# Performance work log

Hardware: AMD Instinct MI355X
Metric: run time of the kernel (lower is better)

Reference implementation:

```python
import jax, jax.numpy as jnp
import numpy as np

EMBED_DIM = 256
NUM_HEADS = 8
HEAD_DIM = EMBED_DIM // NUM_HEADS
SCALE = HEAD_DIM ** -0.5  # note: scale uses head_dim even though attention is over full D
EPS = 1e-12  # torch F.normalize eps


def setup_inputs() -> dict:
    key = jax.random.key(0)
    k1, k2, k3 = jax.random.split(key, 3)
    B, Nq, Nk, D = 4, 4096, 4096, EMBED_DIM
    return {
        "query": jax.random.normal(k1, (B, Nq, D), dtype=jnp.float32),
        "key": jax.random.normal(k2, (B, Nk, D), dtype=jnp.float32),
        "value": jax.random.normal(k3, (B, Nk, D), dtype=jnp.float32),
    }


def _l2_normalize(x):
    # matches torch.nn.functional.normalize(x, dim=-1): x / max(||x||, eps)
    n = jnp.linalg.norm(x, axis=-1, keepdims=True)
    return x / jnp.maximum(n, EPS)


def reference(query, key, value):
    q = _l2_normalize(query)          # (B, Nq, D)
    k = _l2_normalize(key)            # (B, Nk, D)
    scores = jnp.einsum("bqd,bkd->bqk", q, k) * SCALE  # (B, Nq, Nk) cosine sims
    attn = jax.nn.softmax(scores, axis=-1)
    return jnp.einsum("bqk,bkd->bqd", attn, value)     # (B, Nq, D)
```

## Files before the change

kernel.cpp:

```cpp
#include <hip/hip_runtime.h>


#define NQ 4096
#define DIM 256
#define NROWS 16384
#define BM 64
#define BN 64
#define KSPLIT 2
#define NITER 32
#define PSTRIDE 68

typedef __attribute__((ext_vector_type(8))) short bf16x8;
typedef __attribute__((ext_vector_type(4))) float f32x4;
typedef __attribute__((ext_vector_type(16))) float f32x16;

__device__ __forceinline__ unsigned short f2bf(float f) {
  unsigned int u = __float_as_uint(f);
  u += 0x7fffu + ((u >> 16) & 1u);
  return (unsigned short)(u >> 16);
}

__device__ __forceinline__ float bf2f(unsigned short h) {
  return __uint_as_float((unsigned int)h << 16);
}

__device__ __forceinline__ unsigned int pack2bf(float a, float b) {
  unsigned int ua = __float_as_uint(a) + 0x8000u;
  unsigned int ub = __float_as_uint(b) + 0x8000u;
  return __builtin_amdgcn_perm(ub, ua, 0x07060302u);
}

__device__ __forceinline__ void gload16(const void* g, void* l) {
  __builtin_amdgcn_global_load_lds(
      (const __attribute__((address_space(1))) unsigned int*)g,
      (__attribute__((address_space(3))) unsigned int*)l, 16, 0, 0);
}

__global__ __launch_bounds__(256) void prep(
    const float* __restrict__ K, const float* __restrict__ V,
    unsigned short* __restrict__ Kfm, unsigned short* __restrict__ Vfm)
{
  __shared__ unsigned short vt[32 * 264];
  const int blk = blockIdx.x, tid = threadIdx.x;
  const int wave = tid >> 6, lane = tid & 63;
  if (blk < 512) {
    const int kt2 = blk;
    const int kt = kt2 >> 1, h = kt2 & 1;
    #pragma unroll
    for (int i = 0; i < 8; i++) {
      const int r = wave*8 + i;
      float4 v = *(const float4*)(K + ((size_t)kt2*32 + r) * DIM + lane * 4);
      float ss = v.x*v.x + v.y*v.y + v.z*v.z + v.w*v.w;
      #pragma unroll
      for (int off = 1; off < 64; off <<= 1) ss += __shfl_xor(ss, off, 64);
      float scale = 1.0f / fmaxf(sqrtf(ss), 1e-12f);
      ushort4 o;
      o.x = f2bf(v.x*scale); o.y = f2bf(v.y*scale);
      o.z = f2bf(v.z*scale); o.w = f2bf(v.w*scale);
      *(ushort4*)(vt + r*264 + lane*4) = o;
    }
    __syncthreads();
    #pragma unroll
    for (int s = 0; s < 4; s++) {
      const int ch = tid + 256*s;
      const int c = ch >> 5, r = ch & 31;
      const int n = h*32 + r;
      bf16x8 val = *(const bf16x8*)(vt + r*264 + c*8);
      *(bf16x8*)(Kfm + (size_t)kt*16384 + (size_t)(c*64 + n)*8) = val;
    }
  } else {
    const int NS = blk - 512;
    #pragma unroll
    for (int i = 0; i < 4; i++) {
      const int e = tid + 256*i;
      const int nl = e >> 6, d = (e & 63) * 4;
      float4 v = *(const float4*)(V + ((size_t)NS*16 + nl)*DIM + d);
      ushort4 o;
      o.x = f2bf(v.x); o.y = f2bf(v.y); o.z = f2bf(v.z); o.w = f2bf(v.w);
      *(ushort4*)(vt + nl*264 + d) = o;
    }
    __syncthreads();
    #pragma unroll
    for (int i = 0; i < 2; i++) {
      const int ch = tid + 256*i;
      const int db = ch >> 6, ln = ch & 63;
      const int row0 = (ln >> 5) * 8, dd = db*32 + (ln & 31);
      ushort4 a, b;
      a.x = vt[(row0+0)*264 + dd]; a.y = vt[(row0+1)*264 + dd];
      a.z = vt[(row0+2)*264 + dd]; a.w = vt[(row0+3)*264 + dd];
      b.x = vt[(row0+4)*264 + dd]; b.y = vt[(row0+5)*264 + dd];
      b.z = vt[(row0+6)*264 + dd]; b.w = vt[(row0+7)*264 + dd];
      size_t base = ((size_t)(NS*8 + db)*64 + ln)*8;
      *(ushort4*)(Vfm + base)     = a;
      *(ushort4*)(Vfm + base + 4) = b;
    }
  }
}

__global__ __launch_bounds__(256, 2) void attn(
    const float* __restrict__ Qg,
    const unsigned short* __restrict__ Kfm,
    const unsigned short* __restrict__ Vfm,
    unsigned short* __restrict__ Opart, float* __restrict__ lpart)
{
  __shared__ unsigned short Klds[32 * 64 * 8];
  __shared__ unsigned short Plds[BM * PSTRIDE];

  const int tid = threadIdx.x, wave = tid >> 6, lane = tid & 63;
  const int l15 = lane & 15, l4 = lane >> 4;
  const int blk = blockIdx.x;
  const int g = blk & 7, qt = blk >> 3;
  const int b = g >> 1, ks = g & 1;
  const int Rq0 = b*NQ + qt*BM;
  const int n0base = b*NQ + ks*(NQ/KSPLIT);
  const int mi = wave & 1, ni = wave >> 1;

  {
    unsigned short* Qlds = Klds;
    #pragma unroll
    for (int i = 0; i < 16; i++) {
      const int r = wave*16 + i;
      float4 v = *(const float4*)(Qg + (size_t)(Rq0 + r)*DIM + lane*4);
      float ss = v.x*v.x + v.y*v.y + v.z*v.z + v.w*v.w;
      #pragma unroll
      for (int off = 1; off < 64; off <<= 1) ss += __shfl_xor(ss, off, 64);
      float scale = (0.17677669529663687f * 1.4426950408889634f)
                    / fmaxf(sqrtf(ss), 1e-12f);
      ushort4 o;
      o.x = f2bf(v.x*scale); o.y = f2bf(v.y*scale);
      o.z = f2bf(v.z*scale); o.w = f2bf(v.w*scale);
      *(ushort4*)(Qlds + r*DIM + lane*4) = o;
    }
  }
  __syncthreads();

  bf16x8 qf[2][8];
  #pragma unroll
  for (int mt = 0; mt < 2; mt++) {
    const unsigned short* qrow = Klds + (mi*32 + mt*16 + l15)*DIM + l4*8;
    #pragma unroll
    for (int kg = 0; kg < 8; kg++)
      qf[mt][kg] = *(const bf16x8*)(qrow + kg*32);
  }
  __syncthreads();

  f32x16 oacc[2][2] = {};
  float lacc[2] = {};

  auto stage = [&](int kt) {
    const unsigned short* src = Kfm + (size_t)((n0base + kt*BN) >> 6) * (32*64*8);
    #pragma unroll
    for (int jj = 0; jj < 4; jj++) {
      const int c = wave*8 + jj*2;
      gload16(src + (size_t)c*512 + lane*8,     Klds + (size_t)c*512);
      gload16(src + (size_t)(c+1)*512 + lane*8, Klds + (size_t)(c+1)*512);
    }
  };

  stage(0);

  for (int kt = 0; kt < NITER; kt++) {
    __syncthreads();

    f32x4 sacc[2][2] = {};
    #pragma unroll
    for (int kg = 0; kg < 8; kg++) {
      bf16x8 kf[2];
      #pragma unroll
      for (int nt = 0; nt < 2; nt++) {
        const int nrow = ni*32 + nt*16 + l15;
        const int c = kg*4 + l4;
        kf[nt] = *(const bf16x8*)(Klds + ((size_t)(c*64 + nrow))*8);
      }
      #pragma unroll
      for (int nt = 0; nt < 2; nt++)
        #pragma unroll
        for (int mt = 0; mt < 2; mt++)
          sacc[nt][mt] = __builtin_amdgcn_mfma_f32_16x16x32_bf16(
              kf[nt], qf[mt][kg], sacc[nt][mt], 0, 0, 0);
    }

    #pragma unroll
    for (int nt = 0; nt < 2; nt++)
      #pragma unroll
      for (int mt = 0; mt < 2; mt++) {
        float p0 = __builtin_amdgcn_exp2f(sacc[nt][mt][0]);
        float p1 = __builtin_amdgcn_exp2f(sacc[nt][mt][1]);
        float p2 = __builtin_amdgcn_exp2f(sacc[nt][mt][2]);
        float p3 = __builtin_amdgcn_exp2f(sacc[nt][mt][3]);
        lacc[mt] += (p0 + p1) + (p2 + p3);
        uint2 pk;
        pk.x = pack2bf(p0, p1);
        pk.y = pack2bf(p2, p3);
        const int m = mi*32 + mt*16 + l15;
        const int n = ni*32 + nt*16 + 4*l4;
        *(uint2*)(Plds + m*PSTRIDE + n) = pk;
      }

    __syncthreads();

    if (kt + 1 < NITER) stage(kt + 1);

    const int NB0 = (n0base + kt*BN) >> 4;
    #pragma unroll
    for (int kstep = 0; kstep < 4; kstep++) {
      bf16x8 pf[2], vf[2];
      #pragma unroll
      for (int mt2 = 0; mt2 < 2; mt2++)
        pf[mt2] = *(const bf16x8*)(Plds + (mt2*32 + (lane & 31))*PSTRIDE
                                   + kstep*16 + 8*(lane >> 5));
      #pragma unroll
      for (int dt = 0; dt < 2; dt++) {
        const int db = wave*2 + dt;
        vf[dt] = *(const bf16x8*)(Vfm + ((size_t)((NB0 + kstep)*8 + db)*64 + lane)*8);
      }
      #pragma unroll
      for (int mt2 = 0; mt2 < 2; mt2++)
        #pragma unroll
        for (int dt = 0; dt < 2; dt++)
          oacc[mt2][dt] = __builtin_amdgcn_mfma_f32_32x32x16_bf16(
              pf[mt2], vf[dt], oacc[mt2][dt], 0, 0, 0);
    }
  }

  #pragma unroll
  for (int mt = 0; mt < 2; mt++) {
    float s = lacc[mt];
    s += __shfl_xor(s, 16, 64);
    s += __shfl_xor(s, 32, 64);
    if (l4 == 0)
      lpart[(size_t)(ks*2 + ni)*NROWS + Rq0 + mi*32 + mt*16 + l15] = s;
  }

  #pragma unroll
  for (int mt2 = 0; mt2 < 2; mt2++)
    #pragma unroll
    for (int dt = 0; dt < 2; dt++)
      #pragma unroll
      for (int reg = 0; reg < 16; reg++) {
        const int m = mt2*32 + 4*(lane >> 5) + (reg & 3) + 8*(reg >> 2);
        const int d = wave*64 + dt*32 + (lane & 31);
        Opart[((size_t)(ks*NROWS + Rq0 + m))*DIM + d] = f2bf(oacc[mt2][dt][reg]);
      }
}

__global__ __launch_bounds__(256) void combine(
    const unsigned short* __restrict__ Opart, const float* __restrict__ lpart,
    float* __restrict__ out)
{
  const size_t idx = (size_t)blockIdx.x*256 + threadIdx.x;
  const size_t e = idx*4;
  const int R = (int)(e >> 8);
  ushort4 o0 = *(const ushort4*)(Opart + e);
  ushort4 o1 = *(const ushort4*)(Opart + (size_t)NROWS*DIM + e);
  float ls = lpart[R] + lpart[NROWS + R] + lpart[2*NROWS + R] + lpart[3*NROWS + R];
  float inv = 1.0f / ls;
  float4 o;
  o.x = (bf2f(o0.x) + bf2f(o1.x))*inv;
  o.y = (bf2f(o0.y) + bf2f(o1.y))*inv;
  o.z = (bf2f(o0.z) + bf2f(o1.z))*inv;
  o.w = (bf2f(o0.w) + bf2f(o1.w))*inv;
  *(float4*)(out + e) = o;
}

extern "C" void kernel_launch(void* const* d_in, const int* in_sizes, int n_in,
                              void* d_out, int out_size, void* d_ws, size_t ws_size,
                              hipStream_t stream) {
  const float* Q = (const float*)d_in[0];
  const float* K = (const float*)d_in[1];
  const float* V = (const float*)d_in[2];
  char* ws = (char*)d_ws;
  unsigned short* Kfm   = (unsigned short*)(ws);
  unsigned short* Vfm   = (unsigned short*)(ws + 8388608);
  unsigned short* Opart = (unsigned short*)(ws + 16777216);
  float* lpart = (float*)(ws + 33554432);

  prep<<<1536, 256, 0, stream>>>(K, V, Kfm, Vfm);
  attn<<<512, 256, 0, stream>>>(Q, Kfm, Vfm, Opart, lpart);
  combine<<<4096, 256, 0, stream>>>(Opart, lpart, (float*)d_out);
}
```

Baseline: 174.6 us.

## Halve query tile to 32 rows, raise occupancy, add MFMA priority hints

Shrinks the query tile from 64 to 32 rows per block, doubling the grid to 1024 blocks and cutting the accumulator and Q-fragment registers so launch bounds can request 4 blocks per CU. Each wave now handles one 16-row slice of scores and one 32-row output tile. s_setprio is raised around the MFMA sequences to favour matrix issue among co-resident waves. The aim is better latency hiding and CU fill. The cost is that every K/V tile is reloaded twice as often per query row, which doubles K/V traffic from L2 and HBM and lowers MFMA work per LDS load.

New measurement: 192.1 us. +10.0%, slower.

```diff
diff --git a/kernel.cpp b/kernel.cpp
--- a/kernel.cpp
+++ b/kernel.cpp
@@ -4,7 +4,7 @@
 #define NQ 4096
 #define DIM 256
 #define NROWS 16384
-#define BM 64
+#define BM 32
 #define BN 64
 #define KSPLIT 2
 #define NITER 32
@@ -97,7 +97,7 @@
   }
 }
 
-__global__ __launch_bounds__(256, 2) void attn(
+__global__ __launch_bounds__(256, 4) void attn(
     const float* __restrict__ Qg,
     const unsigned short* __restrict__ Kfm,
     const unsigned short* __restrict__ Vfm,
@@ -118,8 +118,8 @@
   {
     unsigned short* Qlds = Klds;
     #pragma unroll
-    for (int i = 0; i < 16; i++) {
-      const int r = wave*16 + i;
+    for (int i = 0; i < 8; i++) {
+      const int r = wave*8 + i;
       float4 v = *(const float4*)(Qg + (size_t)(Rq0 + r)*DIM + lane*4);
       float ss = v.x*v.x + v.y*v.y + v.z*v.z + v.w*v.w;
       #pragma unroll
@@ -134,21 +134,20 @@
   }
   __syncthreads();
 
-  bf16x8 qf[2][8];
-  #pragma unroll
-  for (int mt = 0; mt < 2; mt++) {
-    const unsigned short* qrow = Klds + (mi*32 + mt*16 + l15)*DIM + l4*8;
+  bf16x8 qf[8];
+  {
+    const unsigned short* qrow = Klds + (mi*16 + l15)*DIM + l4*8;
     #pragma unroll
     for (int kg = 0; kg < 8; kg++)
-      qf[mt][kg] = *(const bf16x8*)(qrow + kg*32);
+      qf[kg] = *(const bf16x8*)(qrow + kg*32);
   }
   __syncthreads();
 
-  f32x16 oacc[2][2] = {};
-  float lacc[2] = {};
-
-  auto stage = [&](int kt) {
-    const unsigned short* src = Kfm + (size_t)((n0base + kt*BN) >> 6) * (32*64*8);
+  f32x16 oacc[2] = {};
+  float lacc = 0.0f;
+
+  auto stage = [&](int kt_) {
+    const unsigned short* src = Kfm + (size_t)((n0base + kt_*BN) >> 6) * (32*64*8);
     #pragma unroll
     for (int jj = 0; jj < 4; jj++) {
       const int c = wave*8 + jj*2;
@@ -162,7 +161,7 @@
   for (int kt = 0; kt < NITER; kt++) {
     __syncthreads();
 
-    f32x4 sacc[2][2] = {};
+    f32x4 sacc[2] = {};
     #pragma unroll
     for (int kg = 0; kg < 8; kg++) {
       bf16x8 kf[2];
@@ -172,30 +171,28 @@
         const int c = kg*4 + l4;
         kf[nt] = *(const bf16x8*)(Klds + ((size_t)(c*64 + nrow))*8);
       }
+      __builtin_amdgcn_s_setprio(1);
       #pragma unroll
       for (int nt = 0; nt < 2; nt++)
-        #pragma unroll
-        for (int mt = 0; mt < 2; mt++)
-          sacc[nt][mt] = __builtin_amdgcn_mfma_f32_16x16x32_bf16(
-              kf[nt], qf[mt][kg], sacc[nt][mt], 0, 0, 0);
-    }
-
-    #pragma unroll
-    for (int nt = 0; nt < 2; nt++)
-      #pragma unroll
-      for (int mt = 0; mt < 2; mt++) {
-        float p0 = __builtin_amdgcn_exp2f(sacc[nt][mt][0]);
-        float p1 = __builtin_amdgcn_exp2f(sacc[nt][mt][1]);
-        float p2 = __builtin_amdgcn_exp2f(sacc[nt][mt][2]);
-        float p3 = __builtin_amdgcn_exp2f(sacc[nt][mt][3]);
-        lacc[mt] += (p0 + p1) + (p2 + p3);
-        uint2 pk;
-        pk.x = pack2bf(p0, p1);
-        pk.y = pack2bf(p2, p3);
-        const int m = mi*32 + mt*16 + l15;
-        const int n = ni*32 + nt*16 + 4*l4;
-        *(uint2*)(Plds + m*PSTRIDE + n) = pk;
-      }
+        sacc[nt] = __builtin_amdgcn_mfma_f32_16x16x32_bf16(
+            kf[nt], qf[kg], sacc[nt], 0, 0, 0);
+      __builtin_amdgcn_s_setprio(0);
+    }
+
+    #pragma unroll
+    for (int nt = 0; nt < 2; nt++) {
+      float p0 = __builtin_amdgcn_exp2f(sacc[nt][0]);
+      float p1 = __builtin_amdgcn_exp2f(sacc[nt][1]);
+      float p2 = __builtin_amdgcn_exp2f(sacc[nt][2]);
+      float p3 = __builtin_amdgcn_exp2f(sacc[nt][3]);
+      lacc += (p0 + p1) + (p2 + p3);
+      uint2 pk;
+      pk.x = pack2bf(p0, p1);
+      pk.y = pack2bf(p2, p3);
+      const int m = mi*16 + l15;
+      const int n = ni*32 + nt*16 + 4*l4;
+      *(uint2*)(Plds + m*PSTRIDE + n) = pk;
+    }
 
     __syncthreads();
 
@@ -204,44 +201,39 @@
     const int NB0 = (n0base + kt*BN) >> 4;
     #pragma unroll
     for (int kstep = 0; kstep < 4; kstep++) {
-      bf16x8 pf[2], vf[2];
-      #pragma unroll
-      for (int mt2 = 0; mt2 < 2; mt2++)
-        pf[mt2] = *(const bf16x8*)(Plds + (mt2*32 + (lane & 31))*PSTRIDE
-                                   + kstep*16 + 8*(lane >> 5));
+      bf16x8 pf, vf[2];
+      pf = *(const bf16x8*)(Plds + (lane & 31)*PSTRIDE
+                            + kstep*16 + 8*(lane >> 5));
       #pragma unroll
       for (int dt = 0; dt < 2; dt++) {
         const int db = wave*2 + dt;
         vf[dt] = *(const bf16x8*)(Vfm + ((size_t)((NB0 + kstep)*8 + db)*64 + lane)*8);
       }
-      #pragma unroll
-      for (int mt2 = 0; mt2 < 2; mt2++)
-        #pragma unroll
-        for (int dt = 0; dt < 2; dt++)
-          oacc[mt2][dt] = __builtin_amdgcn_mfma_f32_32x32x16_bf16(
-              pf[mt2], vf[dt], oacc[mt2][dt], 0, 0, 0);
-    }
-  }
-
-  #pragma unroll
-  for (int mt = 0; mt < 2; mt++) {
-    float s = lacc[mt];
+      __builtin_amdgcn_s_setprio(1);
+      #pragma unroll
+      for (int dt = 0; dt < 2; dt++)
+        oacc[dt] = __builtin_amdgcn_mfma_f32_32x32x16_bf16(
+            pf, vf[dt], oacc[dt], 0, 0, 0);
+      __builtin_amdgcn_s_setprio(0);
+    }
+  }
+
+  {
+    float s = lacc;
     s += __shfl_xor(s, 16, 64);
     s += __shfl_xor(s, 32, 64);
     if (l4 == 0)
-      lpart[(size_t)(ks*2 + ni)*NROWS + Rq0 + mi*32 + mt*16 + l15] = s;
+      lpart[(size_t)(ks*2 + ni)*NROWS + Rq0 + mi*16 + l15] = s;
   }
 
   #pragma unroll
-  for (int mt2 = 0; mt2 < 2; mt2++)
-    #pragma unroll
-    for (int dt = 0; dt < 2; dt++)
-      #pragma unroll
-      for (int reg = 0; reg < 16; reg++) {
-        const int m = mt2*32 + 4*(lane >> 5) + (reg & 3) + 8*(reg >> 2);
-        const int d = wave*64 + dt*32 + (lane & 31);
-        Opart[((size_t)(ks*NROWS + Rq0 + m))*DIM + d] = f2bf(oacc[mt2][dt][reg]);
-      }
+  for (int dt = 0; dt < 2; dt++)
+    #pragma unroll
+    for (int reg = 0; reg < 16; reg++) {
+      const int m = 4*(lane >> 5) + (reg & 3) + 8*(reg >> 2);
+      const int d = wave*64 + dt*32 + (lane & 31);
+      Opart[((size_t)(ks*NROWS + Rq0 + m))*DIM + d] = f2bf(oacc[dt][reg]);
+    }
 }
 
 __global__ __launch_bounds__(256) void combine(
@@ -276,6 +268,6 @@
   float* lpart = (float*)(ws + 33554432);
 
   prep<<<1536, 256, 0, stream>>>(K, V, Kfm, Vfm);
-  attn<<<512, 256, 0, stream>>>(Q, Kfm, Vfm, Opart, lpart);
+  attn<<<1024, 256, 0, stream>>>(Q, Kfm, Vfm, Opart, lpart);
   combine<<<4096, 256, 0, stream>>>(Opart, lpart, (float*)d_out);
 }
```
